# Kernel tuning notes

Hardware: AMD Instinct MI355X
Metric: run time of the kernel (lower is better)

Reference implementation:

```python
import jax, jax.numpy as jnp
import numpy as np

B, NPG, DEG = 512, 128, 16          # graphs, nodes/graph, out-degree
N = B * NPG                          # 65536 nodes
E = N * DEG                          # 1048576 edges
IN_DIM, HID, HEADS = 11, 32, 4
K1 = int(np.ceil(0.8 * NPG))         # 103 nodes/graph after pool1
K2 = int(np.ceil(0.8 * K1))          # 83 nodes/graph after pool2


def gat_conv(x, src, dst, mask, W, a_s, a_d, b, n_nodes):
    # PyG GATConv (concat=True, add_self_loops=True, eval mode -> no dropout)
    xp = (x @ W).reshape(n_nodes, HEADS, HID)            # [N,H,C]
    as_ = jnp.einsum('nhc,hc->nh', xp, a_s)
    ad_ = jnp.einsum('nhc,hc->nh', xp, a_d)
    loop = jnp.arange(n_nodes)
    s = jnp.concatenate([src, loop])
    d = jnp.concatenate([dst, loop])
    m = jnp.concatenate([mask, jnp.ones(n_nodes, bool)])
    logit = jax.nn.leaky_relu(as_[s] + ad_[d], 0.2)      # [E+N,H]
    logit = jnp.where(m[:, None], logit, -1e9)
    mx = jax.ops.segment_max(logit, d, num_segments=n_nodes)
    ex = jnp.exp(logit - mx[d]) * m[:, None]
    den = jax.ops.segment_sum(ex, d, num_segments=n_nodes)
    alpha = ex / (den[d] + 1e-16)                        # segment softmax over dst
    out = jax.ops.segment_sum(alpha[:, :, None] * xp[s], d, num_segments=n_nodes)
    return out.reshape(n_nodes, HEADS * HID) + b


def topk_pool(x, src, dst, mask, w, npg, k):
    # PyG TopKPooling: score = tanh((x*w).sum(-1)/||w||); keep top ceil(ratio*n) per graph
    nb = x.shape[0] // npg
    score = jnp.tanh((x @ w) / jnp.linalg.norm(w))
    vals, idx = jax.lax.top_k(score.reshape(nb, npg), k)  # [B,k]
    perm = (idx + (jnp.arange(nb) * npg)[:, None]).reshape(-1)
    x_new = x[perm] * vals.reshape(-1, 1)
    remap = jnp.full(nb * npg, -1).at[perm].set(jnp.arange(nb * k))
    ns, nd = remap[src], remap[dst]
    m = mask & (ns >= 0) & (nd >= 0)
    return x_new, jnp.where(m, ns, 0), jnp.where(m, nd, 0), m


def setup_inputs():
    key = jax.random.key(0)
    ks = jax.random.split(key, 24)
    s = 0.05
    x = jax.random.normal(ks[0], (N, IN_DIM), jnp.float32)
    src = jnp.repeat(jnp.arange(N), DEG)
    dst = (src // NPG) * NPG + jax.random.randint(ks[1], (E,), 0, NPG)
    edge_index = jnp.stack([src, dst])
    edge_attr = jax.random.normal(ks[2], (E, 4), jnp.float32)
    batch = jnp.repeat(jnp.arange(B), NPG)
    p = dict(
        W_g1=jax.random.normal(ks[3], (IN_DIM, HEADS * HID), jnp.float32) * s,
        att_src1=jax.random.normal(ks[4], (HEADS, HID), jnp.float32) * s,
        att_dst1=jax.random.normal(ks[5], (HEADS, HID), jnp.float32) * s,
        b_g1=jnp.zeros((HEADS * HID,), jnp.float32),
        W_t1=jax.random.normal(ks[6], (HEADS * HID, HID), jnp.float32) * s,
        b_t1=jnp.zeros((HID,), jnp.float32),
        pool_w1=jax.random.normal(ks[7], (HID,), jnp.float32) * s,
        W_g2=jax.random.normal(ks[8], (HID, HEADS * HID), jnp.float32) * s,
        att_src2=jax.random.normal(ks[9], (HEADS, HID), jnp.float32) * s,
        att_dst2=jax.random.normal(ks[10], (HEADS, HID), jnp.float32) * s,
        b_g2=jnp.zeros((HEADS * HID,), jnp.float32),
        W_t2=jax.random.normal(ks[11], (HEADS * HID, HID), jnp.float32) * s,
        b_t2=jnp.zeros((HID,), jnp.float32),
        pool_w2=jax.random.normal(ks[12], (HID,), jnp.float32) * s,
        W_l1=jax.random.normal(ks[13], (2 * HID, 256), jnp.float32) * s,
        b_l1=jnp.zeros((256,), jnp.float32),
        W_l2=jax.random.normal(ks[14], (256, 1024), jnp.float32) * s,
        b_l2=jnp.zeros((1024,), jnp.float32),
        W_l3=jax.random.normal(ks[15], (1024, 1), jnp.float32) * s,
        b_l3=jnp.zeros((1,), jnp.float32),
    )
    return dict(x=x, edge_index=edge_index, edge_attr=edge_attr, batch=batch, **p)


def reference(x, edge_index, edge_attr, batch,
              W_g1, att_src1, att_dst1, b_g1, W_t1, b_t1, pool_w1,
              W_g2, att_src2, att_dst2, b_g2, W_t2, b_t2, pool_w2,
              W_l1, b_l1, W_l2, b_l2, W_l3, b_l3):
    # edge_attr is ignored (GATConv built without edge_dim); batch is implicit
    # in the fixed equal-size graph layout.  Eval mode -> dropout disabled.
    src, dst = edge_index[0], edge_index[1]
    mask = jnp.ones(E, bool)
    h = jax.nn.relu(gat_conv(x, src, dst, mask, W_g1, att_src1, att_dst1, b_g1, N))
    h = h @ W_t1 + b_t1
    h, src, dst, mask = topk_pool(h, src, dst, mask, pool_w1, NPG, K1)
    h1 = h.reshape(B, K1, HID)
    g1 = jnp.concatenate([h1.max(1), h1.mean(1)], axis=1)   # [B, 2*HID]
    h = jax.nn.relu(gat_conv(h, src, dst, mask, W_g2, att_src2, att_dst2, b_g2, B * K1))
    h = h @ W_t2 + b_t2
    h, src, dst, mask = topk_pool(h, src, dst, mask, pool_w2, K1, K2)
    h2 = h.reshape(B, K2, HID)
    g2 = jnp.concatenate([h2.max(1), h2.mean(1)], axis=1)
    g = g1 + g2
    g = jax.nn.relu(g @ W_l1 + b_l1)
    g = jax.nn.relu(g @ W_l2 + b_l2)
    return g @ W_l3 + b_l3                                   # [B,1]
```

## Files before the change

kernel.cpp:

```cpp
#include <hip/hip_runtime.h>
#include <math.h>

constexpr int NPGc  = 128;
constexpr int NG    = 512;
constexpr int EPGc  = 2048;
constexpr int ETOT  = 1048576;
constexpr int IND   = 11;
constexpr int HIDc  = 32;
constexpr int FD    = 128;
constexpr int K1c   = 103;
constexpr int K2c   = 83;
constexpr int NN    = NG * NPGc;
constexpr int N2c   = NG * K1c;
constexpr int EPAD  = 2432;
constexpr int SBCAP = 2560;
constexpr int OFFSTR= 264;

__device__ __forceinline__ float lrelu(float x){ return fmaxf(x, 0.2f*x); }

template<int KIN>
__device__ void foldDev(const float* __restrict__ Wg, const float* __restrict__ avs,
                        const float* __restrict__ avd, float* __restrict__ S, float* __restrict__ D, int t)
{
    if (t < KIN * 4) {
        int k = t >> 2, h = t & 3;
        float s = 0.f, d = 0.f;
        for (int j = 0; j < HIDc; j++) {
            float w = Wg[k*FD + h*HIDc + j];
            s = fmaf(w, avs[h*HIDc + j], s);
            d = fmaf(w, avd[h*HIDc + j], d);
        }
        S[t] = s; D[t] = d;
    }
}

__global__ __launch_bounds__(256) void k_prep(const int* __restrict__ ei,
    const float* __restrict__ W1g, const float* __restrict__ s1, const float* __restrict__ d1,
    const float* __restrict__ W2g, const float* __restrict__ s2, const float* __restrict__ d2,
    int* __restrict__ csrOff, unsigned char* __restrict__ csrSB,
    float* __restrict__ S1, float* __restrict__ D1, float* __restrict__ S2, float* __restrict__ D2)
{
    int b = blockIdx.x, t = threadIdx.x;
    if (b >= NG) {
        if (b == NG)     foldDev<IND>(W1g, s1, d1, S1, D1, t);
        else             foldDev<HIDc>(W2g, s2, d2, S2, D2, t);
        return;
    }
    int g = b;
    __shared__ int cnt[128], cur[128], offL[129];
    __shared__ __align__(16) unsigned char sbL[SBCAP];
    if (t < 128) cnt[t] = 0;
    if (t < SBCAP/16) ((int4*)sbL)[t] = make_int4(0,0,0,0);
    __syncthreads();
    const int* dstG = ei + ETOT + g * EPGc;
    int dnv[8];
    #pragma unroll
    for (int q = 0; q < 8; q++) {
        int e = t + 256*q;
        dnv[q] = dstG[e] - g * NPGc;
        atomicAdd(&cnt[dnv[q]], 1);
    }
    __syncthreads();
    if (t < 64) {
        int c0 = cnt[2*t], c1 = cnt[2*t + 1];
        int p0 = (c0 + 3) & ~3, p1 = (c1 + 3) & ~3;
        int ps = p0 + p1, P = ps;
        #pragma unroll
        for (int dl = 1; dl < 64; dl <<= 1) { int v = __shfl_up(P, dl); if (t >= dl) P += v; }
        int E0 = P - ps;
        offL[2*t] = E0; offL[2*t + 1] = E0 + p0;
        cur[2*t]  = E0; cur[2*t + 1]  = E0 + p0;
        if (t == 63) offL[128] = P;
    }
    __syncthreads();
    #pragma unroll
    for (int q = 0; q < 8; q++) {
        int e = t + 256*q;
        int pos = atomicAdd(&cur[dnv[q]], 1);
        sbL[pos] = (unsigned char)(e >> 4);
    }
    __syncthreads();
    if (t < SBCAP/16) ((int4*)(csrSB + (size_t)g * SBCAP))[t] = ((const int4*)sbL)[t];
    if (t <= 128) csrOff[g*OFFSTR + t] = offL[t];
    if (t < 128)  csrOff[g*OFFSTR + 132 + t] = cur[t];
}

template<int NNODE, int KIN>
__global__ __launch_bounds__(256) void k_gat(
    const float* __restrict__ xin, const float* __restrict__ Wg,
    const float* __restrict__ WsS, const float* __restrict__ WsD,
    const int* __restrict__ csrOff, const unsigned char* __restrict__ csrSB,
    const float* __restrict__ bias, const float* __restrict__ Wt,
    float* __restrict__ htp)
{
    int g = blockIdx.x, h = blockIdx.y, t = threadIdx.x;
    constexpr int UN = (NNODE*KIN > EPAD ? NNODE*KIN : EPAD);
    __shared__ __align__(16) float xpL[NNODE * 32];
    __shared__ __align__(16) float uni[UN];
    __shared__ __align__(16) unsigned char sbL[SBCAP];
    __shared__ float asL[NNODE], adL[NNODE], sfW[NNODE], sDen[NNODE];
    __shared__ unsigned short offL[NNODE + 1], endL[NNODE];
    __shared__ float WsSL[KIN], WsDL[KIN], bL[32];

    float* xF  = uni;
    float* wEL = uni;

    float wcol[KIN];
    {
        const float* wg = Wg + h*32 + (t & 31);
        #pragma unroll
        for (int k = 0; k < KIN; k++) wcol[k] = wg[k*FD];
    }
    {
        const float* xg = xin + (size_t)g * NNODE * KIN;
        constexpr int XF4 = NNODE * KIN / 4;
        for (int i = t; i < XF4; i += 256) ((float4*)xF)[i] = ((const float4*)xg)[i];
    }
    if (t < KIN) { WsSL[t] = WsS[t*4 + h]; WsDL[t] = WsD[t*4 + h]; }
    if (t < 32) bL[t] = bias[h*32 + t];
    if (t <= NNODE) offL[t] = (unsigned short)csrOff[g*OFFSTR + t];
    if (t < NNODE)  endL[t] = (unsigned short)csrOff[g*OFFSTR + 132 + t];
    if (t < SBCAP/16) ((int4*)sbL)[t] = ((const int4*)(csrSB + (size_t)g * SBCAP))[t];
    __syncthreads();

    {
        const int c = t & 31, r0 = t >> 5;
        const int c4v = c >> 2, csw = c & 3;
        for (int r = r0; r < NNODE; r += 8) {
            const float* xr = xF + r * KIN;
            float acc = 0.f;
            #pragma unroll
            for (int k = 0; k < KIN; k++) acc = fmaf(xr[k], wcol[k], acc);
            xpL[r*32 + (((c4v ^ (r & 7)) << 2) | csw)] = acc;
        }
    }
    if (t < NNODE) {
        const float* xr = xF + t * KIN;
        float s = 0.f, d = 0.f;
        #pragma unroll
        for (int k = 0; k < KIN; k++) { float v = xr[k]; s = fmaf(v, WsSL[k], s); d = fmaf(v, WsDL[k], d); }
        asL[t] = s; adL[t] = d;
    }
    __syncthreads();

    if (t < NNODE) {
        float as_n = asL[t], adn = adL[t];
        int lo = offL[t], er = endL[t], hp = offL[t + 1];
        float mx = as_n;
        int i = lo;
        for (; i + 4 <= er; i += 4) {
            unsigned int q4 = *(const unsigned int*)(sbL + i);
            float a0 = asL[q4 & 255], a1 = asL[(q4 >> 8) & 255];
            float a2 = asL[(q4 >> 16) & 255], a3 = asL[q4 >> 24];
            mx = fmaxf(fmaxf(fmaxf(fmaxf(mx, a0), a1), a2), a3);
        }
        for (; i < er; i++) mx = fmaxf(mx, asL[sbL[i]]);
        float m = lrelu(mx + adn);
        float ws = expf(lrelu(as_n + adn) - m);
        float den = ws;
        i = lo;
        for (; i + 4 <= er; i += 4) {
            unsigned int q4 = *(const unsigned int*)(sbL + i);
            float w0 = expf(lrelu(asL[q4 & 255] + adn) - m);
            float w1 = expf(lrelu(asL[(q4 >> 8) & 255] + adn) - m);
            float w2 = expf(lrelu(asL[(q4 >> 16) & 255] + adn) - m);
            float w3 = expf(lrelu(asL[q4 >> 24] + adn) - m);
            *(float4*)(wEL + i) = make_float4(w0, w1, w2, w3);
            den += w0; den += w1; den += w2; den += w3;
        }
        for (; i < er; i++) {
            float w = expf(lrelu(asL[sbL[i]] + adn) - m);
            wEL[i] = w; den += w;
        }
        for (; i < hp; i++) wEL[i] = 0.f;
        sfW[t] = ws; sDen[t] = den;
    }
    __syncthreads();

    const float4* X4 = (const float4*)xpL;
    float4 rv[4];
    #pragma unroll
    for (int r = 0; r < 4; r++) {
        int p = t + r*256;
        if (p < NNODE * 8) {
            int n = p >> 3, c4 = p & 7;
            float w0 = sfW[n];
            float4 v = X4[n*8 + (c4 ^ (n & 7))];
            float4 a; a.x = w0*v.x; a.y = w0*v.y; a.z = w0*v.z; a.w = w0*v.w;
            int lo = offL[n], hi = offL[n + 1];
            for (int s = lo; s < hi; s += 4) {
                unsigned int q4 = *(const unsigned int*)(sbL + s);
                float4 w4 = *(const float4*)(wEL + s);
                int s0 = q4 & 255;         float4 u0 = X4[s0*8 + (c4 ^ (s0 & 7))];
                a.x = fmaf(w4.x, u0.x, a.x); a.y = fmaf(w4.x, u0.y, a.y);
                a.z = fmaf(w4.x, u0.z, a.z); a.w = fmaf(w4.x, u0.w, a.w);
                int s1 = (q4 >> 8) & 255;  float4 u1 = X4[s1*8 + (c4 ^ (s1 & 7))];
                a.x = fmaf(w4.y, u1.x, a.x); a.y = fmaf(w4.y, u1.y, a.y);
                a.z = fmaf(w4.y, u1.z, a.z); a.w = fmaf(w4.y, u1.w, a.w);
                int s2 = (q4 >> 16) & 255; float4 u2 = X4[s2*8 + (c4 ^ (s2 & 7))];
                a.x = fmaf(w4.z, u2.x, a.x); a.y = fmaf(w4.z, u2.y, a.y);
                a.z = fmaf(w4.z, u2.z, a.z); a.w = fmaf(w4.z, u2.w, a.w);
                int s3 = q4 >> 24;         float4 u3 = X4[s3*8 + (c4 ^ (s3 & 7))];
                a.x = fmaf(w4.w, u3.x, a.x); a.y = fmaf(w4.w, u3.y, a.y);
                a.z = fmaf(w4.w, u3.z, a.z); a.w = fmaf(w4.w, u3.w, a.w);
            }
            float inv = 1.f / (sDen[n] + 1e-16f);
            rv[r].x = fmaxf(fmaf(a.x, inv, bL[c4*4 + 0]), 0.f);
            rv[r].y = fmaxf(fmaf(a.y, inv, bL[c4*4 + 1]), 0.f);
            rv[r].z = fmaxf(fmaf(a.z, inv, bL[c4*4 + 2]), 0.f);
            rv[r].w = fmaxf(fmaf(a.w, inv, bL[c4*4 + 3]), 0.f);
        }
    }
    __syncthreads();
    {
        float4* X4w = (float4*)xpL;
        #pragma unroll
        for (int r = 0; r < 4; r++) {
            int p = t + r*256;
            if (p < NNODE * 8) {
                int n = p >> 3, c4 = p & 7;
                X4w[n*8 + (c4 ^ (n & 7))] = rv[r];
            }
        }
    }
    __syncthreads();

    const int n0 = t >> 3, j4 = t & 7;
    const float* WtH = Wt + h*1024 + j4*4;
    float4 a0 = make_float4(0,0,0,0), a1 = a0, a2 = a0, a3 = a0;
    #pragma unroll
    for (int c4 = 0; c4 < 8; c4++) {
        const int sw = c4 ^ (n0 & 7);
        float4 x0 = X4[n0*8 + sw];
        float4 x1 = make_float4(0,0,0,0), x2v = x1, x3 = x1;
        if (n0 + 32 < NNODE) x1  = X4[(n0+32)*8 + sw];
        if (n0 + 64 < NNODE) x2v = X4[(n0+64)*8 + sw];
        if (n0 + 96 < NNODE) x3  = X4[(n0+96)*8 + sw];
        const float e0[4] = {x0.x, x0.y, x0.z, x0.w};
        const float e1[4] = {x1.x, x1.y, x1.z, x1.w};
        const float e2[4] = {x2v.x, x2v.y, x2v.z, x2v.w};
        const float e3[4] = {x3.x, x3.y, x3.z, x3.w};
        #pragma unroll
        for (int j = 0; j < 4; j++) {
            float4 w4 = *(const float4*)(WtH + (c4*4 + j)*32);
            a0.x = fmaf(e0[j], w4.x, a0.x); a0.y = fmaf(e0[j], w4.y, a0.y);
            a0.z = fmaf(e0[j], w4.z, a0.z); a0.w = fmaf(e0[j], w4.w, a0.w);
            a1.x = fmaf(e1[j], w4.x, a1.x); a1.y = fmaf(e1[j], w4.y, a1.y);
            a1.z = fmaf(e1[j], w4.z, a1.z); a1.w = fmaf(e1[j], w4.w, a1.w);
            a2.x = fmaf(e2[j], w4.x, a2.x); a2.y = fmaf(e2[j], w4.y, a2.y);
            a2.z = fmaf(e2[j], w4.z, a2.z); a2.w = fmaf(e2[j], w4.w, a2.w);
            a3.x = fmaf(e3[j], w4.x, a3.x); a3.y = fmaf(e3[j], w4.y, a3.y);
            a3.z = fmaf(e3[j], w4.z, a3.z); a3.w = fmaf(e3[j], w4.w, a3.w);
        }
    }
    {
        size_t base = ((size_t)(g * NNODE + n0) * 4 + h) * 32 + j4 * 4;
        *(float4*)(htp + base) = a0;
        if (n0 + 32 < NNODE) *(float4*)(htp + base + (size_t)32*128) = a1;
        if (n0 + 64 < NNODE) *(float4*)(htp + base + (size_t)64*128) = a2;
        if (n0 + 96 < NNODE) *(float4*)(htp + base + (size_t)96*128) = a3;
    }
}

template<int NIN, int KEEP, bool FIRST>
__global__ __launch_bounds__(256) void k_linpool(
    const float* __restrict__ htp, const float* __restrict__ bt, const float* __restrict__ pw,
    float* __restrict__ xnew, const int* __restrict__ ei,
    int* __restrict__ csrOffW, unsigned char* __restrict__ sbW,
    float* __restrict__ gfeat, const float* __restrict__ gprev,
    const float* __restrict__ W1, const float* __restrict__ b1,
    const float* __restrict__ W2, const float* __restrict__ b2,
    const float* __restrict__ W3, const float* __restrict__ b3,
    float* __restrict__ outp)
{
    int g = blockIdx.x, t = threadIdx.x;
    __shared__ float htL[NIN * 33];
    __shared__ float scoreL[NIN];
    __shared__ int rnkL[NIN];
    __shared__ int cnt[128], cur[128], offL[129];
    __shared__ __align__(16) unsigned char sbL[SBCAP];
    __shared__ float gvec[64];
    __shared__ float h1L[256], red[256];

    for (int p = t; p < NIN * 8; p += 256) {
        int n = p >> 3, q = p & 7;
        const float4* row = (const float4*)(htp + (size_t)(g * NIN + n) * 128);
        float4 s = ((const float4*)bt)[q];
        float4 p0 = row[q], p1 = row[8 + q], p2 = row[16 + q], p3 = row[24 + q];
        s.x += p0.x; s.y += p0.y; s.z += p0.z; s.w += p0.w;
        s.x += p1.x; s.y += p1.y; s.z += p1.z; s.w += p1.w;
        s.x += p2.x; s.y += p2.y; s.z += p2.z; s.w += p2.w;
        s.x += p3.x; s.y += p3.y; s.z += p3.z; s.w += p3.w;
        float* d = htL + n*33 + q*4;
        d[0] = s.x; d[1] = s.y; d[2] = s.z; d[3] = s.w;
    }
    __syncthreads();

    float nrm; { float ss = 0.f; for (int k = 0; k < HIDc; k++) { float w = pw[k]; ss = fmaf(w, w, ss); } nrm = sqrtf(ss); }
    if (t < NIN) {
        float dot = 0.f;
        for (int k = 0; k < HIDc; k++) dot = fmaf(htL[t*33 + k], pw[k], dot);
        scoreL[t] = tanhf(dot / nrm);
    }
    __syncthreads();
    if (t < NIN) {
        float si = scoreL[t]; int rank = 0;
        for (int q = 0; q < NIN; q++) {
            float sj = scoreL[q];
            rank += (sj > si || (sj == si && q < t)) ? 1 : 0;
        }
        rnkL[t] = (rank < KEEP) ? rank : -1;
    }
    __syncthreads();
    if constexpr (FIRST) {
        for (int p = t; p < NIN * 32; p += 256) {
            int n = p >> 5, jj = p & 31;
            int rk = rnkL[n];
            if (rk >= 0) xnew[((size_t)g*KEEP + rk)*HIDc + jj] = htL[n*33 + jj] * scoreL[n];
        }
    }
    if (t < HIDc) {
        float mx = -INFINITY, sm = 0.f;
        for (int n = 0; n < NIN; n++) {
            if (rnkL[n] >= 0) { float v = htL[n*33 + t] * scoreL[n]; mx = fmaxf(mx, v); sm += v; }
        }
        float mean = sm / (float)KEEP;
        if constexpr (FIRST) {
            gfeat[(size_t)g*64 + t]      = mx;
            gfeat[(size_t)g*64 + 32 + t] = mean;
        } else {
            gvec[t]      = gprev[(size_t)g*64 + t] + mx;
            gvec[32 + t] = gprev[(size_t)g*64 + 32 + t] + mean;
        }
    }

    if constexpr (FIRST) {
        __syncthreads();
        if (t < 128) cnt[t] = 0;
        if (t < SBCAP/16) ((int4*)sbL)[t] = make_int4(0,0,0,0);
        __syncthreads();
        const int* dstG = ei + ETOT + g * EPGc;
        int snv[8], dnv[8];
        #pragma unroll
        for (int q = 0; q < 8; q++) {
            int e = t + 256*q;
            int s = rnkL[e >> 4], d = rnkL[dstG[e] - g * NPGc];
            bool ok = (s >= 0 && d >= 0);
            snv[q] = s; dnv[q] = ok ? d : -1;
            if (ok) atomicAdd(&cnt[d], 1);
        }
        __syncthreads();
        if (t < 64) {
            int c0 = cnt[2*t], c1 = cnt[2*t + 1];
            int p0 = (c0 + 3) & ~3, p1 = (c1 + 3) & ~3;
            int ps = p0 + p1, P = ps;
            #pragma unroll
            for (int dl = 1; dl < 64; dl <<= 1) { int v = __shfl_up(P, dl); if (t >= dl) P += v; }
            int E0 = P - ps;
            offL[2*t] = E0; offL[2*t + 1] = E0 + p0;
            cur[2*t]  = E0; cur[2*t + 1]  = E0 + p0;
            if (t == 63) offL[128] = P;
        }
        __syncthreads();
        #pragma unroll
        for (int q = 0; q < 8; q++) {
            if (dnv[q] >= 0) {
                int pos = atomicAdd(&cur[dnv[q]], 1);
                sbL[pos] = (unsigned char)snv[q];
            }
        }
        __syncthreads();
        if (t < SBCAP/16) ((int4*)(sbW + (size_t)g * SBCAP))[t] = ((const int4*)sbL)[t];
        if (t <= K1c) csrOffW[g*OFFSTR + t] = offL[t];
        if (t < K1c)  csrOffW[g*OFFSTR + 132 + t] = cur[t];
    } else {
        __syncthreads();
        float a = b1[t];
        #pragma unroll 4
        for (int k = 0; k < 64; k++) a = fmaf(gvec[k], W1[k*256 + t], a);
        h1L[t] = fmaxf(a, 0.f);
        __syncthreads();
        float c0 = b2[t], c1 = b2[t + 256], c2 = b2[t + 512], c3 = b2[t + 768];
        const float* w2c = W2 + t;
        #pragma unroll 4
        for (int i = 0; i < 256; i++) {
            float hv = h1L[i];
            const float* wr = w2c + (size_t)i * 1024;
            c0 = fmaf(hv, wr[0],   c0);
            c1 = fmaf(hv, wr[256], c1);
            c2 = fmaf(hv, wr[512], c2);
            c3 = fmaf(hv, wr[768], c3);
        }
        float p = fmaf(fmaxf(c0, 0.f), W3[t],
                  fmaf(fmaxf(c1, 0.f), W3[t + 256],
                  fmaf(fmaxf(c2, 0.f), W3[t + 512],
                       fmaxf(c3, 0.f) * W3[t + 768])));
        red[t] = p;
        __syncthreads();
        for (int s = 128; s > 0; s >>= 1) { if (t < s) red[t] += red[t + s]; __syncthreads(); }
        if (t == 0) outp[g] = red[0] + b3[0];
    }
}

extern "C" void kernel_launch(void* const* d_in, const int* in_sizes, int n_in,
                              void* d_out, int out_size, void* d_ws, size_t ws_size,
                              hipStream_t stream)
{
    const float* x    = (const float*)d_in[0];
    const int*   ei   = (const int*)  d_in[1];
    const float* W_g1 = (const float*)d_in[4];
    const float* as1w = (const float*)d_in[5];
    const float* ad1w = (const float*)d_in[6];
    const float* b_g1 = (const float*)d_in[7];
    const float* W_t1 = (const float*)d_in[8];
    const float* b_t1 = (const float*)d_in[9];
    const float* pw1  = (const float*)d_in[10];
    const float* W_g2 = (const float*)d_in[11];
    const float* as2w = (const float*)d_in[12];
    const float* ad2w = (const float*)d_in[13];
    const float* b_g2 = (const float*)d_in[14];
    const float* W_t2 = (const float*)d_in[15];
    const float* b_t2 = (const float*)d_in[16];
    const float* pw2  = (const float*)d_in[17];
    const float* W_l1 = (const float*)d_in[18];
    const float* b_l1 = (const float*)d_in[19];
    const float* W_l2 = (const float*)d_in[20];
    const float* b_l2 = (const float*)d_in[21];
    const float* W_l3 = (const float*)d_in[22];
    const float* b_l3 = (const float*)d_in[23];
    float* out = (float*)d_out;

    char* ws = (char*)d_ws;
    size_t off = 0;
    auto alloc = [&](size_t bytes) -> void* {
        void* p = (void*)(ws + off);
        off += ((bytes + 255) / 256) * 256;
        return p;
    };
    float* htp1  = (float*)alloc((size_t)NN * 128 * 4);
    float* htp2  = (float*)alloc((size_t)N2c * 128 * 4);
    float* x2    = (float*)alloc((size_t)N2c * HIDc * 4);
    float* g1    = (float*)alloc((size_t)NG * 64 * 4);
    float* wsS1  = (float*)alloc(64 * 4);
    float* wsD1  = (float*)alloc(64 * 4);
    float* wsS2  = (float*)alloc(128 * 4);
    float* wsD2  = (float*)alloc(128 * 4);
    int*   off1  = (int*)  alloc((size_t)NG * OFFSTR * 4);
    unsigned char* sb1 = (unsigned char*)alloc((size_t)NG * SBCAP);
    int*   off2  = (int*)  alloc((size_t)NG * OFFSTR * 4);
    unsigned char* sb2 = (unsigned char*)alloc((size_t)NG * SBCAP);

    k_prep<<<NG + 2, 256, 0, stream>>>(ei, W_g1, as1w, ad1w, W_g2, as2w, ad2w,
                                       off1, sb1, wsS1, wsD1, wsS2, wsD2);

    k_gat<NPGc, IND><<<dim3(NG, 4), 256, 0, stream>>>(
        x, W_g1, wsS1, wsD1, off1, sb1, b_g1, W_t1, htp1);

    k_linpool<NPGc, K1c, true><<<NG, 256, 0, stream>>>(
        htp1, b_t1, pw1, x2, ei, off2, sb2, g1, nullptr,
        nullptr, nullptr, nullptr, nullptr, nullptr, nullptr, nullptr);

    k_gat<K1c, HIDc><<<dim3(NG, 4), 256, 0, stream>>>(
        x2, W_g2, wsS2, wsD2, off2, sb2, b_g2, W_t2, htp2);

    k_linpool<K1c, K2c, false><<<NG, 256, 0, stream>>>(
        htp2, b_t2, pw2, nullptr, nullptr, nullptr, nullptr, nullptr, g1,
        W_l1, b_l1, W_l2, b_l2, W_l3, b_l3, out);
}
```

Before: 298.5 us.

## Recompute attention weights in aggregation and pad CSR with sentinel node

Drops the per-edge attention weight buffer in shared memory and recomputes exp(leaky_relu) for each edge during aggregation, keeping only the per-node max and inverse denominator. CSR padding slots now point to a sentinel node index (128 or 103) whose source score is -1e30, so padded edges give zero weight without separate tail loops or end offsets. The GEMM reads x directly from global memory with W staged in shared memory. This cuts shared memory use and loop overhead, likely improving occupancy, but every edge's exp is now computed 8 times (once per float4 lane group) instead of once.

```diff
diff --git a/kernel.cpp b/kernel.cpp
--- a/kernel.cpp
+++ b/kernel.cpp
@@ -49,8 +49,9 @@
     int g = b;
     __shared__ int cnt[128], cur[128], offL[129];
     __shared__ __align__(16) unsigned char sbL[SBCAP];
+    const int FILL1 = (int)0x80808080u;
     if (t < 128) cnt[t] = 0;
-    if (t < SBCAP/16) ((int4*)sbL)[t] = make_int4(0,0,0,0);
+    if (t < SBCAP/16) ((int4*)sbL)[t] = make_int4(FILL1, FILL1, FILL1, FILL1);
     __syncthreads();
     const int* dstG = ei + ETOT + g * EPGc;
     int dnv[8];
@@ -94,86 +95,62 @@
     float* __restrict__ htp)
 {
     int g = blockIdx.x, h = blockIdx.y, t = threadIdx.x;
-    constexpr int UN = (NNODE*KIN > EPAD ? NNODE*KIN : EPAD);
     __shared__ __align__(16) float xpL[NNODE * 32];
-    __shared__ __align__(16) float uni[UN];
+    __shared__ __align__(16) float WL[KIN * 32];
     __shared__ __align__(16) unsigned char sbL[SBCAP];
-    __shared__ float asL[NNODE], adL[NNODE], sfW[NNODE], sDen[NNODE];
-    __shared__ unsigned short offL[NNODE + 1], endL[NNODE];
-    __shared__ float WsSL[KIN], WsDL[KIN], bL[32];
-
-    float* xF  = uni;
-    float* wEL = uni;
-
-    float wcol[KIN];
-    {
-        const float* wg = Wg + h*32 + (t & 31);
-        #pragma unroll
-        for (int k = 0; k < KIN; k++) wcol[k] = wg[k*FD];
-    }
-    {
-        const float* xg = xin + (size_t)g * NNODE * KIN;
-        constexpr int XF4 = NNODE * KIN / 4;
-        for (int i = t; i < XF4; i += 256) ((float4*)xF)[i] = ((const float4*)xg)[i];
-    }
-    if (t < KIN) { WsSL[t] = WsS[t*4 + h]; WsDL[t] = WsD[t*4 + h]; }
-    if (t < 32) bL[t] = bias[h*32 + t];
+    __shared__ float asL[NNODE + 1], adL[NNODE], mL[NNODE], dIL[NNODE];
+    __shared__ unsigned short offL[NNODE + 1];
+
+    const float* xg = xin + (size_t)g * NNODE * KIN;
+
+    for (int i = t; i < KIN * 32; i += 256) { int k = i >> 5, c = i & 31; WL[i] = Wg[k*FD + h*32 + c]; }
     if (t <= NNODE) offL[t] = (unsigned short)csrOff[g*OFFSTR + t];
-    if (t < NNODE)  endL[t] = (unsigned short)csrOff[g*OFFSTR + 132 + t];
     if (t < SBCAP/16) ((int4*)sbL)[t] = ((const int4*)(csrSB + (size_t)g * SBCAP))[t];
-    __syncthreads();
-
-    {
-        const int c = t & 31, r0 = t >> 5;
-        const int c4v = c >> 2, csw = c & 3;
-        for (int r = r0; r < NNODE; r += 8) {
-            const float* xr = xF + r * KIN;
-            float acc = 0.f;
-            #pragma unroll
-            for (int k = 0; k < KIN; k++) acc = fmaf(xr[k], wcol[k], acc);
-            xpL[r*32 + (((c4v ^ (r & 7)) << 2) | csw)] = acc;
-        }
+    if (t == NNODE) asL[NNODE] = -1e30f;
+    __syncthreads();
+
+    for (int p = t; p < NNODE * 8; p += 256) {
+        int n = p >> 3, c4 = p & 7;
+        const float* xr = xg + (size_t)n * KIN;
+        float4 acc = make_float4(0.f, 0.f, 0.f, 0.f);
+        #pragma unroll
+        for (int k = 0; k < KIN; k++) {
+            float xv = xr[k];
+            float4 w4 = *(const float4*)&WL[k*32 + c4*4];
+            acc.x = fmaf(xv, w4.x, acc.x); acc.y = fmaf(xv, w4.y, acc.y);
+            acc.z = fmaf(xv, w4.z, acc.z); acc.w = fmaf(xv, w4.w, acc.w);
+        }
+        ((float4*)xpL)[n*8 + (c4 ^ (n & 7))] = acc;
     }
     if (t < NNODE) {
-        const float* xr = xF + t * KIN;
+        const float* xr = xg + (size_t)t * KIN;
         float s = 0.f, d = 0.f;
         #pragma unroll
-        for (int k = 0; k < KIN; k++) { float v = xr[k]; s = fmaf(v, WsSL[k], s); d = fmaf(v, WsDL[k], d); }
+        for (int k = 0; k < KIN; k++) { float v = xr[k]; s = fmaf(v, WsS[k*4 + h], s); d = fmaf(v, WsD[k*4 + h], d); }
         asL[t] = s; adL[t] = d;
     }
     __syncthreads();
 
     if (t < NNODE) {
         float as_n = asL[t], adn = adL[t];
-        int lo = offL[t], er = endL[t], hp = offL[t + 1];
+        int lo = offL[t], hi = offL[t + 1];
         float mx = as_n;
-        int i = lo;
-        for (; i + 4 <= er; i += 4) {
+        for (int i = lo; i < hi; i += 4) {
             unsigned int q4 = *(const unsigned int*)(sbL + i);
             float a0 = asL[q4 & 255], a1 = asL[(q4 >> 8) & 255];
             float a2 = asL[(q4 >> 16) & 255], a3 = asL[q4 >> 24];
             mx = fmaxf(fmaxf(fmaxf(fmaxf(mx, a0), a1), a2), a3);
         }
-        for (; i < er; i++) mx = fmaxf(mx, asL[sbL[i]]);
         float m = lrelu(mx + adn);
-        float ws = expf(lrelu(as_n + adn) - m);
-        float den = ws;
-        i = lo;
-        for (; i + 4 <= er; i += 4) {
+        float den = expf(lrelu(as_n + adn) - m);
+        for (int i = lo; i < hi; i += 4) {
             unsigned int q4 = *(const unsigned int*)(sbL + i);
-            float w0 = expf(lrelu(asL[q4 & 255] + adn) - m);
-            float w1 = expf(lrelu(asL[(q4 >> 8) & 255] + adn) - m);
-            float w2 = expf(lrelu(asL[(q4 >> 16) & 255] + adn) - m);
-            float w3 = expf(lrelu(asL[q4 >> 24] + adn) - m);
-            *(float4*)(wEL + i) = make_float4(w0, w1, w2, w3);
-            den += w0; den += w1; den += w2; den += w3;
-        }
-        for (; i < er; i++) {
-            float w = expf(lrelu(asL[sbL[i]] + adn) - m);
-            wEL[i] = w; den += w;
-        }
-        for (; i < hp; i++) wEL[i] = 0.f;
-        sfW[t] = ws; sDen[t] = den;
+            den += expf(lrelu(asL[q4 & 255] + adn) - m);
+            den += expf(lrelu(asL[(q4 >> 8) & 255] + adn) - m);
+            den += expf(lrelu(asL[(q4 >> 16) & 255] + adn) - m);
+            den += expf(lrelu(asL[q4 >> 24] + adn) - m);
+        }
+        mL[t] = m; dIL[t] = 1.f / (den + 1e-16f);
     }
     __syncthreads();
 
@@ -184,31 +161,39 @@
         int p = t + r*256;
         if (p < NNODE * 8) {
             int n = p >> 3, c4 = p & 7;
-            float w0 = sfW[n];
+            float adn = adL[n], mn = mL[n];
+            float w0 = expf(lrelu(asL[n] + adn) - mn);
             float4 v = X4[n*8 + (c4 ^ (n & 7))];
             float4 a; a.x = w0*v.x; a.y = w0*v.y; a.z = w0*v.z; a.w = w0*v.w;
             int lo = offL[n], hi = offL[n + 1];
             for (int s = lo; s < hi; s += 4) {
                 unsigned int q4 = *(const unsigned int*)(sbL + s);
-                float4 w4 = *(const float4*)(wEL + s);
-                int s0 = q4 & 255;         float4 u0 = X4[s0*8 + (c4 ^ (s0 & 7))];
-                a.x = fmaf(w4.x, u0.x, a.x); a.y = fmaf(w4.x, u0.y, a.y);
-                a.z = fmaf(w4.x, u0.z, a.z); a.w = fmaf(w4.x, u0.w, a.w);
-                int s1 = (q4 >> 8) & 255;  float4 u1 = X4[s1*8 + (c4 ^ (s1 & 7))];
-                a.x = fmaf(w4.y, u1.x, a.x); a.y = fmaf(w4.y, u1.y, a.y);
-                a.z = fmaf(w4.y, u1.z, a.z); a.w = fmaf(w4.y, u1.w, a.w);
-                int s2 = (q4 >> 16) & 255; float4 u2 = X4[s2*8 + (c4 ^ (s2 & 7))];
-                a.x = fmaf(w4.z, u2.x, a.x); a.y = fmaf(w4.z, u2.y, a.y);
-                a.z = fmaf(w4.z, u2.z, a.z); a.w = fmaf(w4.z, u2.w, a.w);
-                int s3 = q4 >> 24;         float4 u3 = X4[s3*8 + (c4 ^ (s3 & 7))];
-                a.x = fmaf(w4.w, u3.x, a.x); a.y = fmaf(w4.w, u3.y, a.y);
-                a.z = fmaf(w4.w, u3.z, a.z); a.w = fmaf(w4.w, u3.w, a.w);
+                int s0 = q4 & 255, s1 = (q4 >> 8) & 255, s2 = (q4 >> 16) & 255, s3 = q4 >> 24;
+                float e0 = expf(lrelu(asL[s0] + adn) - mn);
+                float e1 = expf(lrelu(asL[s1] + adn) - mn);
+                float e2 = expf(lrelu(asL[s2] + adn) - mn);
+                float e3 = expf(lrelu(asL[s3] + adn) - mn);
+                int r0 = min(s0, NNODE-1), r1 = min(s1, NNODE-1);
+                int r2 = min(s2, NNODE-1), r3 = min(s3, NNODE-1);
+                float4 u0 = X4[r0*8 + (c4 ^ (r0 & 7))];
+                a.x = fmaf(e0, u0.x, a.x); a.y = fmaf(e0, u0.y, a.y);
+                a.z = fmaf(e0, u0.z, a.z); a.w = fmaf(e0, u0.w, a.w);
+                float4 u1 = X4[r1*8 + (c4 ^ (r1 & 7))];
+                a.x = fmaf(e1, u1.x, a.x); a.y = fmaf(e1, u1.y, a.y);
+                a.z = fmaf(e1, u1.z, a.z); a.w = fmaf(e1, u1.w, a.w);
+                float4 u2 = X4[r2*8 + (c4 ^ (r2 & 7))];
+                a.x = fmaf(e2, u2.x, a.x); a.y = fmaf(e2, u2.y, a.y);
+                a.z = fmaf(e2, u2.z, a.z); a.w = fmaf(e2, u2.w, a.w);
+                float4 u3 = X4[r3*8 + (c4 ^ (r3 & 7))];
+                a.x = fmaf(e3, u3.x, a.x); a.y = fmaf(e3, u3.y, a.y);
+                a.z = fmaf(e3, u3.z, a.z); a.w = fmaf(e3, u3.w, a.w);
             }
-            float inv = 1.f / (sDen[n] + 1e-16f);
-            rv[r].x = fmaxf(fmaf(a.x, inv, bL[c4*4 + 0]), 0.f);
-            rv[r].y = fmaxf(fmaf(a.y, inv, bL[c4*4 + 1]), 0.f);
-            rv[r].z = fmaxf(fmaf(a.z, inv, bL[c4*4 + 2]), 0.f);
-            rv[r].w = fmaxf(fmaf(a.w, inv, bL[c4*4 + 3]), 0.f);
+            float inv = dIL[n];
+            float4 bq = *(const float4*)(bias + h*32 + c4*4);
+            rv[r].x = fmaxf(fmaf(a.x, inv, bq.x), 0.f);
+            rv[r].y = fmaxf(fmaf(a.y, inv, bq.y), 0.f);
+            rv[r].z = fmaxf(fmaf(a.z, inv, bq.z), 0.f);
+            rv[r].w = fmaxf(fmaf(a.w, inv, bq.w), 0.f);
         }
     }
     __syncthreads();
@@ -336,8 +321,9 @@
 
     if constexpr (FIRST) {
         __syncthreads();
+        const int FILL2 = (int)0x67676767u;
         if (t < 128) cnt[t] = 0;
-        if (t < SBCAP/16) ((int4*)sbL)[t] = make_int4(0,0,0,0);
+        if (t < SBCAP/16) ((int4*)sbL)[t] = make_int4(FILL2, FILL2, FILL2, FILL2);
         __syncthreads();
         const int* dstG = ei + ETOT + g * EPGc;
         int snv[8], dnv[8];
```

Result: slower. 322.8 us (+8.2%).
